# Performance work log

Hardware: AMD Instinct MI355X
Metric: run time of the kernel (lower is better)

Reference implementation:

```python
import jax, jax.numpy as jnp
import numpy as np

DIM, HEADS, K = 128, 4, 7
HD = DIM // HEADS


def _nbr_idx(n, k):
    # NATTEN boundary-clamped neighborhood (dilation=1): window start clamped to [0, n-k]
    i = np.arange(n)
    start = np.clip(i - k // 2, 0, n - k)
    idx = start[:, None] + np.arange(k)[None, :]          # (n, k) absolute neighbor index
    rel = idx - i[:, None] + (k - 1)                      # (n, k) index into 2k-1 rpb axis
    return jnp.asarray(idx), jnp.asarray(rel)


def _ln(x, w, b, eps=1e-5):
    mu = jnp.mean(x, -1, keepdims=True)
    var = jnp.var(x, -1, keepdims=True)
    return (x - mu) * jax.lax.rsqrt(var + eps) * w + b


def setup_inputs() -> dict:
    key = jax.random.key(0)
    ks = jax.random.split(key, 16)
    B, H, W, C = 1, 128, 128, DIM
    f = jax.random.normal
    inp = {
        'x': f(ks[0], (B, H, W, C), jnp.float32),
        'y': f(ks[1], (B, H, W, C), jnp.float32),
        'qv_w': f(ks[2], (2 * C, C), jnp.float32) * 0.02,
        'qv_b': jnp.zeros((2 * C,), jnp.float32),
        'k_w': f(ks[3], (C, C), jnp.float32) * 0.02,
        'k_b': jnp.zeros((C,), jnp.float32),
        'rpb': f(ks[4], (HEADS, 2 * K - 1, 2 * K - 1), jnp.float32) * 0.02,
        'proj_w': f(ks[5], (C, C), jnp.float32) * 0.02,
        'proj_b': jnp.zeros((C,), jnp.float32),
        'n1_w': jnp.ones((C,), jnp.float32),
        'n1_b': jnp.zeros((C,), jnp.float32),
        'n2_w': jnp.ones((C,), jnp.float32),
        'n2_b': jnp.zeros((C,), jnp.float32),
        'fc1_w': f(ks[6], (4 * C, C), jnp.float32) * 0.02,
        'fc1_b': jnp.zeros((4 * C,), jnp.float32),
        'fc2_w': f(ks[7], (C, 4 * C), jnp.float32) * 0.02,
        'fc2_b': jnp.zeros((C,), jnp.float32),
    }
    return inp


def _block(x, y, qv_w, qv_b, k_w, k_b, rpb, proj_w, proj_b,
           n1_w, n1_b, n2_w, n2_b, fc1_w, fc1_b, fc2_w, fc2_b):
    B, H, W, C = x.shape
    scale = HD ** -0.5
    # ---- CrossNat2D attention on norm1(x) vs y ----
    xn = _ln(x, n1_w, n1_b)
    qv = xn @ qv_w.T + qv_b                               # (B,H,W,2C)
    q = qv[..., :C].reshape(B, H, W, HEADS, HD) * scale
    v = qv[..., C:].reshape(B, H, W, HEADS, HD)
    k = (y @ k_w.T + k_b).reshape(B, H, W, HEADS, HD)

    idx_h, rel_h = _nbr_idx(H, K)
    idx_w, rel_w = _nbr_idx(W, K)
    # gather neighborhoods: (B, H, K, W, K, HEADS, HD)
    k_nbr = k[:, idx_h][:, :, :, idx_w]
    v_nbr = v[:, idx_h][:, :, :, idx_w]

    # attention logits over KxK neighborhood
    attn = jnp.einsum('bijhd,biajchd->bijhac', q, k_nbr)  # (B,H,W,heads,K,K)
    bias = rpb[:, rel_h][..., rel_w]                      # (heads,H,K,W,K)
    attn = attn + jnp.transpose(bias, (1, 3, 0, 2, 4))    # broadcast over B
    attn = jax.nn.softmax(attn.reshape(B, H, W, HEADS, K * K), axis=-1)
    attn = attn.reshape(B, H, W, HEADS, K, K)

    out = jnp.einsum('bijhac,biajchd->bijhd', attn, v_nbr).reshape(B, H, W, C)
    out = out @ proj_w.T + proj_b

    x = x + out
    # ---- MLP ----
    h = _ln(x, n2_w, n2_b) @ fc1_w.T + fc1_b
    h = jax.nn.gelu(h, approximate=False) @ fc2_w.T + fc2_b
    return x + h


def reference(x, y, qv_w, qv_b, k_w, k_b, rpb, proj_w, proj_b,
              n1_w, n1_b, n2_w, n2_b, fc1_w, fc1_b, fc2_w, fc2_b):
    return _block(x, y, qv_w, qv_b, k_w, k_b, rpb, proj_w, proj_b,
                  n1_w, n1_b, n2_w, n2_b, fc1_w, fc1_b, fc2_w, fc2_b)
```

## Files before the change

### kernel.cpp

```cpp
#include <hip/hip_runtime.h>
#include <hip/hip_bf16.h>


#define N_PIX 16384
#define C 128
#define HEADS 4
#define HD 32
#define HW 128

typedef __hip_bfloat16 bf16;
typedef __attribute__((ext_vector_type(8))) short bf16x8;
typedef __attribute__((ext_vector_type(4))) float f32x4;

__device__ __forceinline__ short f2bs(float f) {
    bf16 h = __float2bfloat16(f);
    return (short)__bfloat16_as_ushort(h);
}
__device__ __forceinline__ float bs2f(short s) {
    __hip_bfloat16_raw r; r.x = (unsigned short)s;
    return __bfloat162float(__hip_bfloat16(r));
}
__device__ __forceinline__ float gelu_f(float v) {
    const float z = 1.5957691216f * (v + 0.044715f * v * v * v);
    return v / (1.f + __expf(-z));
}

__global__ __launch_bounds__(256) void k_wconv(
    const float* __restrict__ qv_w, const float* __restrict__ k_w,
    const float* __restrict__ proj_w, const float* __restrict__ fc1_w,
    const float* __restrict__ fc2_w,
    short* __restrict__ wqv, short* __restrict__ wk, short* __restrict__ wproj,
    short* __restrict__ wfc1, short* __restrict__ wfc2) {
    const int i = blockIdx.x * 256 + threadIdx.x;
    if (i < 32768) wqv[i] = f2bs(qv_w[i]);
    if (i < 16384) { wk[i] = f2bs(k_w[i]); wproj[i] = f2bs(proj_w[i]); }
    if (i < 65536) { wfc1[i] = f2bs(fc1_w[i]); wfc2[i] = f2bs(fc2_w[i]); }
}

__global__ __launch_bounds__(512, 6) void k_qkv(
    const float* __restrict__ x, const float* __restrict__ y,
    const short* __restrict__ wqv, const float* __restrict__ qv_b,
    const short* __restrict__ wk, const float* __restrict__ k_b,
    const float* __restrict__ n1_w, const float* __restrict__ n1_b,
    bf16* __restrict__ qb, bf16* __restrict__ vb, bf16* __restrict__ kb) {
    __shared__ float xr[32][132];
    __shared__ short xn[32][136];
    __shared__ short yb[32][136];
    __shared__ float muA[32], riA[32];
    const int t = threadIdx.x;
    const int pix0 = (blockIdx.x & 7) * 2048 + (blockIdx.x >> 3) * 32;
    for (int e = t; e < 32 * 128; e += 512) {
        const int r = e >> 7, c = e & 127;
        xr[r][c] = x[(pix0 + r) * C + c];
        yb[r][c] = f2bs(y[(pix0 + r) * C + c]);
    }
    __syncthreads();
    if (t < 256) {
        const int r = t >> 3, s = t & 7;
        float sm = 0.f, sq = 0.f;
        for (int i = 0; i < 16; i++) { float v = xr[r][s * 16 + i]; sm += v; sq += v * v; }
        for (int m = 1; m < 8; m <<= 1) { sm += __shfl_xor(sm, m, 64); sq += __shfl_xor(sq, m, 64); }
        if (s == 0) {
            const float mu = sm * (1.f / 128.f);
            const float var = sq * (1.f / 128.f) - mu * mu;
            muA[r] = mu; riA[r] = rsqrtf(var + 1e-5f);
        }
    }
    __syncthreads();
    for (int e = t; e < 32 * 128; e += 512) {
        const int r = e >> 7, c = e & 127;
        xn[r][c] = f2bs((xr[r][c] - muA[r]) * riA[r] * n1_w[c] + n1_b[c]);
    }
    __syncthreads();
    const int wave = t >> 6, lane = t & 63, quad = lane >> 4, l15 = lane & 15;
    const int mt = wave & 1, wv = wave >> 1;
    const float scale = 0.1767766952966369f;
    {
        bf16x8 aA[4];
#pragma unroll
        for (int kt = 0; kt < 4; kt++)
            aA[kt] = *(const bf16x8*)&xn[mt * 16 + l15][kt * 32 + quad * 8];
#pragma unroll
        for (int s = 0; s < 4; s++) {
            const int n = (wv * 4 + s) * 16 + l15;
            f32x4 acc = {0.f, 0.f, 0.f, 0.f};
#pragma unroll
            for (int kt = 0; kt < 4; kt++) {
                bf16x8 b = *(const bf16x8*)&wqv[n * C + kt * 32 + quad * 8];
                acc = __builtin_amdgcn_mfma_f32_16x16x32_bf16(aA[kt], b, acc, 0, 0, 0);
            }
            const float bias = qv_b[n];
#pragma unroll
            for (int r = 0; r < 4; r++) {
                const int m = mt * 16 + quad * 4 + r;
                const float v = acc[r] + bias;
                if (n < C) qb[(pix0 + m) * C + n] = __float2bfloat16(v * scale);
                else       vb[(pix0 + m) * C + (n - C)] = __float2bfloat16(v);
            }
        }
    }
    {
        bf16x8 aY[4];
#pragma unroll
        for (int kt = 0; kt < 4; kt++)
            aY[kt] = *(const bf16x8*)&yb[mt * 16 + l15][kt * 32 + quad * 8];
        const int n0 = (wv * 2) * 16 + l15, n1 = (wv * 2 + 1) * 16 + l15;
        f32x4 a0 = {0.f, 0.f, 0.f, 0.f}, a1 = {0.f, 0.f, 0.f, 0.f};
#pragma unroll
        for (int kt = 0; kt < 4; kt++) {
            bf16x8 b0 = *(const bf16x8*)&wk[n0 * C + kt * 32 + quad * 8];
            bf16x8 b1 = *(const bf16x8*)&wk[n1 * C + kt * 32 + quad * 8];
            a0 = __builtin_amdgcn_mfma_f32_16x16x32_bf16(aY[kt], b0, a0, 0, 0, 0);
            a1 = __builtin_amdgcn_mfma_f32_16x16x32_bf16(aY[kt], b1, a1, 0, 0, 0);
        }
        const float b0s = k_b[n0], b1s = k_b[n1];
#pragma unroll
        for (int r = 0; r < 4; r++) {
            const int m = mt * 16 + quad * 4 + r;
            kb[(pix0 + m) * C + n0] = __float2bfloat16(a0[r] + b0s);
            kb[(pix0 + m) * C + n1] = __float2bfloat16(a1[r] + b1s);
        }
    }
}

__global__ __launch_bounds__(256) void k_fam(
    const bf16* __restrict__ qb, const bf16* __restrict__ kb,
    const bf16* __restrict__ vb, const float* __restrict__ rpb,
    const float* __restrict__ x,
    const short* __restrict__ wproj, const float* __restrict__ proj_b,
    const float* __restrict__ n2_w, const float* __restrict__ n2_b,
    const short* __restrict__ wfc1, const float* __restrict__ fc1_b,
    const short* __restrict__ wfc2, const float* __restrict__ fc2_b,
    float* __restrict__ out) {
    __shared__ short KP[13200];
    __shared__ short Vl[13200];
    __shared__ float muA[16], riA[16];
    short* const Pm  = KP;
    short* const aoL = KP + 8704;
    short* const x1b = KP + 10880;
    short* const hb  = Vl;
    short* const xnb = Vl + 8320;
    const int t = threadIdx.x;
    const int h = t >> 6, lane = t & 63, quad = lane >> 4, l15 = lane & 15;
    const int s_ = blockIdx.x >> 3;
    const int i0 = ((blockIdx.x & 7) * 4 + (s_ >> 5)) * 4;
    const int j0 = (s_ & 31) * 4;
    const int rs = min(max(i0 - 3, 0), 118);
    const int cs = min(max(j0 - 3, 0), 118);
    for (int u = t; u < 100 * 16 * 2; u += 256) {
        const int tv = (u >= 1600) ? 1 : 0;
        const int uu = tv ? u - 1600 : u;
        const int r = uu >> 4, seg = uu & 15;
        const size_t g = (size_t)((rs + r / 10) * HW + cs + r % 10) * C + seg * 8;
        const uint4 d = *(const uint4*)((tv ? vb : kb) + g);
        *(uint4*)&(tv ? Vl : KP)[r * 132 + seg * 8] = d;
    }
    __syncthreads();
    const int pA = (i0 + (l15 >> 2)) * HW + j0 + (l15 & 3);
    const bf16x8 aQ = *(const bf16x8*)(qb + (size_t)pA * C + h * HD + quad * 8);
    f32x4 S[7];
    int aiL[7], ajL[7]; bool inb[7];
#pragma unroll
    for (int nt = 0; nt < 7; nt++) {
        const int nb = nt * 16 + l15;
        aiL[nt] = rs + nb / 10;
        ajL[nt] = cs + nb % 10;
        inb[nt] = nb < 100;
        const bf16x8 bK = *(const bf16x8*)&KP[(nt * 16 + l15) * 132 + h * HD + quad * 8];
        f32x4 z = {0.f, 0.f, 0.f, 0.f};
        S[nt] = __builtin_amdgcn_mfma_f32_16x16x32_bf16(aQ, bK, z, 0, 0, 0);
    }
    const float* rpbh = rpb + h * 169;
    float smx[4];
#pragma unroll
    for (int r = 0; r < 4; r++) {
        const int m = quad * 4 + r;
        const int i = i0 + (m >> 2), j = j0 + (m & 3);
        const int shi = min(max(i - 3, 0), 121);
        const int swj = min(max(j - 3, 0), 121);
        float best = -1e30f;
#pragma unroll
        for (int nt = 0; nt < 7; nt++) {
            const int ai = aiL[nt], aj = ajL[nt];
            const bool valid = inb[nt] & (ai >= shi) & (ai <= shi + 6) & (aj >= swj) & (aj <= swj + 6);
            const int ri = min(max(ai - i + 6, 0), 12);
            const int rj = min(max(aj - j + 6, 0), 12);
            const float v = valid ? (S[nt][r] + rpbh[ri * 13 + rj]) : -1e30f;
            S[nt][r] = v;
            best = fmaxf(best, v);
        }
        for (int msk = 1; msk < 16; msk <<= 1) best = fmaxf(best, __shfl_xor(best, msk, 64));
        float s = 0.f;
#pragma unroll
        for (int nt = 0; nt < 7; nt++) {
            const float e = __expf(S[nt][r] - best);
            S[nt][r] = e;
            s += e;
        }
        for (int msk = 1; msk < 16; msk <<= 1) s += __shfl_xor(s, msk, 64);
        smx[r] = 1.f / s;
    }
    __syncthreads();
#pragma unroll
    for (int r = 0; r < 4; r++) {
        short* prow = &Pm[(h * 16 + quad * 4 + r) * 136];
#pragma unroll
        for (int nt = 0; nt < 7; nt++)
            prow[nt * 16 + l15] = f2bs(S[nt][r] * smx[r]);
        prow[112 + l15] = 0;
    }
    __syncthreads();
    f32x4 O0 = {0.f, 0.f, 0.f, 0.f}, O1 = {0.f, 0.f, 0.f, 0.f};
#pragma unroll
    for (int kt = 0; kt < 4; kt++) {
        const bf16x8 aP = *(const bf16x8*)&Pm[(h * 16 + l15) * 136 + kt * 32 + quad * 8];
#pragma unroll
        for (int nt2 = 0; nt2 < 2; nt2++) {
            bf16x8 bV;
            const int ch = h * HD + nt2 * 16 + l15;
#pragma unroll
            for (int jj = 0; jj < 8; jj++) {
                const int nbr = kt * 32 + quad * 8 + jj;
                bV[jj] = (nbr < 100) ? Vl[nbr * 132 + ch] : (short)0;
            }
            if (nt2 == 0) O0 = __builtin_amdgcn_mfma_f32_16x16x32_bf16(aP, bV, O0, 0, 0, 0);
            else          O1 = __builtin_amdgcn_mfma_f32_16x16x32_bf16(aP, bV, O1, 0, 0, 0);
        }
    }
#pragma unroll
    for (int r = 0; r < 4; r++) {
        const int m = quad * 4 + r;
        aoL[m * 136 + h * HD + l15] = f2bs(O0[r]);
        aoL[m * 136 + h * HD + 16 + l15] = f2bs(O1[r]);
    }
    __syncthreads();
    {
        bf16x8 aO[4];
#pragma unroll
        for (int kt = 0; kt < 4; kt++)
            aO[kt] = *(const bf16x8*)&aoL[l15 * 136 + kt * 32 + quad * 8];
        const int n0 = h * 16 + l15, n1 = (h + 4) * 16 + l15;
        f32x4 a0 = {0.f, 0.f, 0.f, 0.f}, a1 = {0.f, 0.f, 0.f, 0.f};
#pragma unroll
        for (int kt = 0; kt < 4; kt++) {
            bf16x8 b0 = *(const bf16x8*)&wproj[n0 * C + kt * 32 + quad * 8];
            bf16x8 b1 = *(const bf16x8*)&wproj[n1 * C + kt * 32 + quad * 8];
            a0 = __builtin_amdgcn_mfma_f32_16x16x32_bf16(aO[kt], b0, a0, 0, 0, 0);
            a1 = __builtin_amdgcn_mfma_f32_16x16x32_bf16(aO[kt], b1, a1, 0, 0, 0);
        }
        const float b0s = proj_b[n0], b1s = proj_b[n1];
#pragma unroll
        for (int r = 0; r < 4; r++) {
            const int m = quad * 4 + r;
            const int p = (i0 + (m >> 2)) * HW + j0 + (m & 3);
            x1b[m * 136 + n0] = f2bs(x[(size_t)p * C + n0] + a0[r] + b0s);
            x1b[m * 136 + n1] = f2bs(x[(size_t)p * C + n1] + a1[r] + b1s);
        }
    }
    __syncthreads();
    if (t < 128) {
        const int r = t >> 3, s = t & 7;
        float sm = 0.f, sq = 0.f;
        for (int i = 0; i < 16; i++) { float v = bs2f(x1b[r * 136 + s * 16 + i]); sm += v; sq += v * v; }
        for (int m = 1; m < 8; m <<= 1) { sm += __shfl_xor(sm, m, 64); sq += __shfl_xor(sq, m, 64); }
        if (s == 0) {
            const float mu = sm * (1.f / 128.f);
            const float var = sq * (1.f / 128.f) - mu * mu;
            muA[r] = mu; riA[r] = rsqrtf(var + 1e-5f);
        }
    }
    __syncthreads();
    for (int e = t; e < 16 * 128; e += 256) {
        const int r = e >> 7, c = e & 127;
        xnb[r * 136 + c] = f2bs((bs2f(x1b[r * 136 + c]) - muA[r]) * riA[r] * n2_w[c] + n2_b[c]);
    }
    __syncthreads();
    {
        bf16x8 aX[4];
#pragma unroll
        for (int kt = 0; kt < 4; kt++)
            aX[kt] = *(const bf16x8*)&xnb[l15 * 136 + kt * 32 + quad * 8];
#pragma unroll
        for (int a = 0; a < 4; a++) {
            const int n0 = (h + 8 * a) * 16 + l15, n1 = (h + 8 * a + 4) * 16 + l15;
            f32x4 a0 = {0.f, 0.f, 0.f, 0.f}, a1 = {0.f, 0.f, 0.f, 0.f};
#pragma unroll
            for (int kt = 0; kt < 4; kt++) {
                bf16x8 b0 = *(const bf16x8*)&wfc1[n0 * C + kt * 32 + quad * 8];
                bf16x8 b1 = *(const bf16x8*)&wfc1[n1 * C + kt * 32 + quad * 8];
                a0 = __builtin_amdgcn_mfma_f32_16x16x32_bf16(aX[kt], b0, a0, 0, 0, 0);
                a1 = __builtin_amdgcn_mfma_f32_16x16x32_bf16(aX[kt], b1, a1, 0, 0, 0);
            }
            const float b0s = fc1_b[n0], b1s = fc1_b[n1];
#pragma unroll
            for (int r = 0; r < 4; r++) {
                hb[(quad * 4 + r) * 520 + n0] = f2bs(gelu_f(a0[r] + b0s));
                hb[(quad * 4 + r) * 520 + n1] = f2bs(gelu_f(a1[r] + b1s));
            }
        }
    }
    __syncthreads();
    {
        const int n0 = h * 16 + l15, n1 = (h + 4) * 16 + l15;
        f32x4 a0 = {0.f, 0.f, 0.f, 0.f}, a1 = {0.f, 0.f, 0.f, 0.f};
#pragma unroll
        for (int kt = 0; kt < 16; kt++) {
            const bf16x8 aP = *(const bf16x8*)&hb[l15 * 520 + kt * 32 + quad * 8];
            bf16x8 b0 = *(const bf16x8*)&wfc2[n0 * 512 + kt * 32 + quad * 8];
            bf16x8 b1 = *(const bf16x8*)&wfc2[n1 * 512 + kt * 32 + quad * 8];
            a0 = __builtin_amdgcn_mfma_f32_16x16x32_bf16(aP, b0, a0, 0, 0, 0);
            a1 = __builtin_amdgcn_mfma_f32_16x16x32_bf16(aP, b1, a1, 0, 0, 0);
        }
        const float b0s = fc2_b[n0], b1s = fc2_b[n1];
#pragma unroll
        for (int r = 0; r < 4; r++) {
            const int m = quad * 4 + r;
            const int p = (i0 + (m >> 2)) * HW + j0 + (m & 3);
            out[(size_t)p * C + n0] = a0[r] + b0s + bs2f(x1b[m * 136 + n0]);
            out[(size_t)p * C + n1] = a1[r] + b1s + bs2f(x1b[m * 136 + n1]);
        }
    }
}

extern "C" void kernel_launch(void* const* d_in, const int* in_sizes, int n_in,
                              void* d_out, int out_size, void* d_ws, size_t ws_size,
                              hipStream_t stream) {
    const float* x      = (const float*)d_in[0];
    const float* y      = (const float*)d_in[1];
    const float* qv_w   = (const float*)d_in[2];
    const float* qv_b   = (const float*)d_in[3];
    const float* k_w    = (const float*)d_in[4];
    const float* k_b    = (const float*)d_in[5];
    const float* rpb    = (const float*)d_in[6];
    const float* proj_w = (const float*)d_in[7];
    const float* proj_b = (const float*)d_in[8];
    const float* n1_w   = (const float*)d_in[9];
    const float* n1_b   = (const float*)d_in[10];
    const float* n2_w   = (const float*)d_in[11];
    const float* n2_b   = (const float*)d_in[12];
    const float* fc1_w  = (const float*)d_in[13];
    const float* fc1_b  = (const float*)d_in[14];
    const float* fc2_w  = (const float*)d_in[15];
    const float* fc2_b  = (const float*)d_in[16];
    float* out = (float*)d_out;

    bf16* qb  = (bf16*)d_ws;
    bf16* vb  = qb + (size_t)N_PIX * C;
    bf16* kb  = vb + (size_t)N_PIX * C;
    short* wqv  = (short*)(kb + (size_t)N_PIX * C);
    short* wk   = wqv + 32768;
    short* wproj= wk + 16384;
    short* wfc1 = wproj + 16384;
    short* wfc2 = wfc1 + 65536;

    k_wconv<<<256, 256, 0, stream>>>(qv_w, k_w, proj_w, fc1_w, fc2_w,
                                     wqv, wk, wproj, wfc1, wfc2);
    k_qkv<<<N_PIX / 32, 512, 0, stream>>>(x, y, wqv, qv_b, wk, k_b, n1_w, n1_b, qb, vb, kb);
    k_fam<<<1024, 256, 0, stream>>>(qb, kb, vb, rpb, x, wproj, proj_b, n2_w, n2_b,
                                    wfc1, fc1_b, wfc2, fc2_b, out);
}
```

Baseline: 175.5 us.

## Double per-block pixel tiles in QKV and fused attention-MLP kernels

The QKV projection block now processes 64 pixels instead of 32, and the fused attention/MLP block processes an 8x4 query tile with 512 threads instead of 4x4 with 256. The larger attention tile shares a 14x10 K/V halo across twice the queries, which cuts redundant halo loads and amortises weight fetches per block. In exchange each query scores 144 neighbour slots instead of 112, which is more wasted MFMA work. The grids shrink to 256 and 512 blocks, which lowers occupancy and parallelism on a large GPU. Shared memory is re-laid out, and an extra barrier is added before attention outputs overwrite the probability buffer.

```diff
diff --git a/kernel.cpp b/kernel.cpp
--- a/kernel.cpp
+++ b/kernel.cpp
@@ -37,25 +37,25 @@
     if (i < 65536) { wfc1[i] = f2bs(fc1_w[i]); wfc2[i] = f2bs(fc2_w[i]); }
 }
 
-__global__ __launch_bounds__(512, 6) void k_qkv(
+__global__ __launch_bounds__(512, 2) void k_qkv(
     const float* __restrict__ x, const float* __restrict__ y,
     const short* __restrict__ wqv, const float* __restrict__ qv_b,
     const short* __restrict__ wk, const float* __restrict__ k_b,
     const float* __restrict__ n1_w, const float* __restrict__ n1_b,
     bf16* __restrict__ qb, bf16* __restrict__ vb, bf16* __restrict__ kb) {
-    __shared__ float xr[32][132];
-    __shared__ short xn[32][136];
-    __shared__ short yb[32][136];
-    __shared__ float muA[32], riA[32];
+    __shared__ float xr[64][132];
+    __shared__ short xn[64][136];
+    __shared__ short yb[64][136];
+    __shared__ float muA[64], riA[64];
     const int t = threadIdx.x;
-    const int pix0 = (blockIdx.x & 7) * 2048 + (blockIdx.x >> 3) * 32;
-    for (int e = t; e < 32 * 128; e += 512) {
+    const int pix0 = (blockIdx.x & 7) * 2048 + (blockIdx.x >> 3) * 64;
+    for (int e = t; e < 64 * 128; e += 512) {
         const int r = e >> 7, c = e & 127;
         xr[r][c] = x[(pix0 + r) * C + c];
         yb[r][c] = f2bs(y[(pix0 + r) * C + c]);
     }
     __syncthreads();
-    if (t < 256) {
+    {
         const int r = t >> 3, s = t & 7;
         float sm = 0.f, sq = 0.f;
         for (int i = 0; i < 16; i++) { float v = xr[r][s * 16 + i]; sm += v; sq += v * v; }
@@ -67,13 +67,13 @@
         }
     }
     __syncthreads();
-    for (int e = t; e < 32 * 128; e += 512) {
+    for (int e = t; e < 64 * 128; e += 512) {
         const int r = e >> 7, c = e & 127;
         xn[r][c] = f2bs((xr[r][c] - muA[r]) * riA[r] * n1_w[c] + n1_b[c]);
     }
     __syncthreads();
     const int wave = t >> 6, lane = t & 63, quad = lane >> 4, l15 = lane & 15;
-    const int mt = wave & 1, wv = wave >> 1;
+    const int mt = wave >> 1, half = wave & 1;
     const float scale = 0.1767766952966369f;
     {
         bf16x8 aA[4];
@@ -81,8 +81,8 @@
         for (int kt = 0; kt < 4; kt++)
             aA[kt] = *(const bf16x8*)&xn[mt * 16 + l15][kt * 32 + quad * 8];
 #pragma unroll
-        for (int s = 0; s < 4; s++) {
-            const int n = (wv * 4 + s) * 16 + l15;
+        for (int s = 0; s < 8; s++) {
+            const int n = (half + 2 * s) * 16 + l15;
             f32x4 acc = {0.f, 0.f, 0.f, 0.f};
 #pragma unroll
             for (int kt = 0; kt < 4; kt++) {
@@ -104,26 +104,30 @@
 #pragma unroll
         for (int kt = 0; kt < 4; kt++)
             aY[kt] = *(const bf16x8*)&yb[mt * 16 + l15][kt * 32 + quad * 8];
-        const int n0 = (wv * 2) * 16 + l15, n1 = (wv * 2 + 1) * 16 + l15;
-        f32x4 a0 = {0.f, 0.f, 0.f, 0.f}, a1 = {0.f, 0.f, 0.f, 0.f};
-#pragma unroll
-        for (int kt = 0; kt < 4; kt++) {
-            bf16x8 b0 = *(const bf16x8*)&wk[n0 * C + kt * 32 + quad * 8];
-            bf16x8 b1 = *(const bf16x8*)&wk[n1 * C + kt * 32 + quad * 8];
-            a0 = __builtin_amdgcn_mfma_f32_16x16x32_bf16(aY[kt], b0, a0, 0, 0, 0);
-            a1 = __builtin_amdgcn_mfma_f32_16x16x32_bf16(aY[kt], b1, a1, 0, 0, 0);
-        }
-        const float b0s = k_b[n0], b1s = k_b[n1];
-#pragma unroll
-        for (int r = 0; r < 4; r++) {
-            const int m = mt * 16 + quad * 4 + r;
-            kb[(pix0 + m) * C + n0] = __float2bfloat16(a0[r] + b0s);
-            kb[(pix0 + m) * C + n1] = __float2bfloat16(a1[r] + b1s);
-        }
-    }
-}
-
-__global__ __launch_bounds__(256) void k_fam(
+#pragma unroll
+        for (int s = 0; s < 2; s++) {
+            const int n0 = (half + 2 * (2 * s)) * 16 + l15;
+            const int n1 = (half + 2 * (2 * s + 1)) * 16 + l15;
+            f32x4 a0 = {0.f, 0.f, 0.f, 0.f}, a1 = {0.f, 0.f, 0.f, 0.f};
+#pragma unroll
+            for (int kt = 0; kt < 4; kt++) {
+                bf16x8 b0 = *(const bf16x8*)&wk[n0 * C + kt * 32 + quad * 8];
+                bf16x8 b1 = *(const bf16x8*)&wk[n1 * C + kt * 32 + quad * 8];
+                a0 = __builtin_amdgcn_mfma_f32_16x16x32_bf16(aY[kt], b0, a0, 0, 0, 0);
+                a1 = __builtin_amdgcn_mfma_f32_16x16x32_bf16(aY[kt], b1, a1, 0, 0, 0);
+            }
+            const float b0s = k_b[n0], b1s = k_b[n1];
+#pragma unroll
+            for (int r = 0; r < 4; r++) {
+                const int m = mt * 16 + quad * 4 + r;
+                kb[(pix0 + m) * C + n0] = __float2bfloat16(a0[r] + b0s);
+                kb[(pix0 + m) * C + n1] = __float2bfloat16(a1[r] + b1s);
+            }
+        }
+    }
+}
+
+__global__ __launch_bounds__(512, 2) void k_fam(
     const bf16* __restrict__ qb, const bf16* __restrict__ kb,
     const bf16* __restrict__ vb, const float* __restrict__ rpb,
     const float* __restrict__ x,
@@ -132,57 +136,56 @@
     const short* __restrict__ wfc1, const float* __restrict__ fc1_b,
     const short* __restrict__ wfc2, const float* __restrict__ fc2_b,
     float* __restrict__ out) {
-    __shared__ short KP[13200];
-    __shared__ short Vl[13200];
-    __shared__ float muA[16], riA[16];
+    __shared__ short KP[19008];
+    __shared__ short Vl[19008];
+    __shared__ float muA[32], riA[32];
     short* const Pm  = KP;
-    short* const aoL = KP + 8704;
-    short* const x1b = KP + 10880;
+    short* const aoL = KP;
+    short* const x1b = KP + 4352;
+    short* const xnb = KP + 8704;
     short* const hb  = Vl;
-    short* const xnb = Vl + 8320;
     const int t = threadIdx.x;
-    const int h = t >> 6, lane = t & 63, quad = lane >> 4, l15 = lane & 15;
+    const int wave = t >> 6, lane = t & 63, quad = lane >> 4, l15 = lane & 15;
+    const int h = wave & 3, mt = wave >> 2;
     const int s_ = blockIdx.x >> 3;
-    const int i0 = ((blockIdx.x & 7) * 4 + (s_ >> 5)) * 4;
+    const int i0 = ((blockIdx.x & 7) * 2 + (s_ >> 5)) * 8;
     const int j0 = (s_ & 31) * 4;
-    const int rs = min(max(i0 - 3, 0), 118);
+    const int rs = min(max(i0 - 3, 0), 114);
     const int cs = min(max(j0 - 3, 0), 118);
-    for (int u = t; u < 100 * 16 * 2; u += 256) {
-        const int tv = (u >= 1600) ? 1 : 0;
-        const int uu = tv ? u - 1600 : u;
+    for (int u = t; u < 140 * 16 * 2; u += 512) {
+        const int tv = (u >= 2240) ? 1 : 0;
+        const int uu = tv ? u - 2240 : u;
         const int r = uu >> 4, seg = uu & 15;
         const size_t g = (size_t)((rs + r / 10) * HW + cs + r % 10) * C + seg * 8;
         const uint4 d = *(const uint4*)((tv ? vb : kb) + g);
         *(uint4*)&(tv ? Vl : KP)[r * 132 + seg * 8] = d;
     }
     __syncthreads();
-    const int pA = (i0 + (l15 >> 2)) * HW + j0 + (l15 & 3);
+    const int mA = mt * 16 + l15;
+    const int pA = (i0 + (mA >> 2)) * HW + j0 + (mA & 3);
     const bf16x8 aQ = *(const bf16x8*)(qb + (size_t)pA * C + h * HD + quad * 8);
-    f32x4 S[7];
-    int aiL[7], ajL[7]; bool inb[7];
-#pragma unroll
-    for (int nt = 0; nt < 7; nt++) {
-        const int nb = nt * 16 + l15;
-        aiL[nt] = rs + nb / 10;
-        ajL[nt] = cs + nb % 10;
-        inb[nt] = nb < 100;
+    f32x4 S[9];
+#pragma unroll
+    for (int nt = 0; nt < 9; nt++) {
         const bf16x8 bK = *(const bf16x8*)&KP[(nt * 16 + l15) * 132 + h * HD + quad * 8];
         f32x4 z = {0.f, 0.f, 0.f, 0.f};
         S[nt] = __builtin_amdgcn_mfma_f32_16x16x32_bf16(aQ, bK, z, 0, 0, 0);
     }
+    const int nbL = l15;
     const float* rpbh = rpb + h * 169;
     float smx[4];
 #pragma unroll
     for (int r = 0; r < 4; r++) {
-        const int m = quad * 4 + r;
+        const int m = mt * 16 + quad * 4 + r;
         const int i = i0 + (m >> 2), j = j0 + (m & 3);
         const int shi = min(max(i - 3, 0), 121);
         const int swj = min(max(j - 3, 0), 121);
         float best = -1e30f;
 #pragma unroll
-        for (int nt = 0; nt < 7; nt++) {
-            const int ai = aiL[nt], aj = ajL[nt];
-            const bool valid = inb[nt] & (ai >= shi) & (ai <= shi + 6) & (aj >= swj) & (aj <= swj + 6);
+        for (int nt = 0; nt < 9; nt++) {
+            const int nb = nt * 16 + nbL;
+            const int ai = rs + nb / 10, aj = cs + nb % 10;
+            const bool valid = (nb < 140) & (ai >= shi) & (ai <= shi + 6) & (aj >= swj) & (aj <= swj + 6);
             const int ri = min(max(ai - i + 6, 0), 12);
             const int rj = min(max(aj - j + 6, 0), 12);
             const float v = valid ? (S[nt][r] + rpbh[ri * 13 + rj]) : -1e30f;
@@ -192,7 +195,7 @@
         for (int msk = 1; msk < 16; msk <<= 1) best = fmaxf(best, __shfl_xor(best, msk, 64));
         float s = 0.f;
 #pragma unroll
-        for (int nt = 0; nt < 7; nt++) {
+        for (int nt = 0; nt < 9; nt++) {
             const float e = __expf(S[nt][r] - best);
             S[nt][r] = e;
             s += e;
@@ -203,17 +206,16 @@
     __syncthreads();
 #pragma unroll
     for (int r = 0; r < 4; r++) {
-        short* prow = &Pm[(h * 16 + quad * 4 + r) * 136];
-#pragma unroll
-        for (int nt = 0; nt < 7; nt++)
+        short* prow = &Pm[(wave * 16 + quad * 4 + r) * 144];
+#pragma unroll
+        for (int nt = 0; nt < 9; nt++)
             prow[nt * 16 + l15] = f2bs(S[nt][r] * smx[r]);
-        prow[112 + l15] = 0;
     }
     __syncthreads();
     f32x4 O0 = {0.f, 0.f, 0.f, 0.f}, O1 = {0.f, 0.f, 0.f, 0.f};
 #pragma unroll
-    for (int kt = 0; kt < 4; kt++) {
-        const bf16x8 aP = *(const bf16x8*)&Pm[(h * 16 + l15) * 136 + kt * 32 + quad * 8];
+    for (int kt = 0; kt < 5; kt++) {
+        const bf16x8 aP = *(const bf16x8*)&Pm[(wave * 16 + l15) * 144 + kt * 32 + quad * 8];
 #pragma unroll
         for (int nt2 = 0; nt2 < 2; nt2++) {
             bf16x8 bV;
@@ -221,15 +223,16 @@
 #pragma unroll
             for (int jj = 0; jj < 8; jj++) {
                 const int nbr = kt * 32 + quad * 8 + jj;
-                bV[jj] = (nbr < 100) ? Vl[nbr * 132 + ch] : (short)0;
+                bV[jj] = (nbr < 140) ? Vl[nbr * 132 + ch] : (short)0;
             }
             if (nt2 == 0) O0 = __builtin_amdgcn_mfma_f32_16x16x32_bf16(aP, bV, O0, 0, 0, 0);
             else          O1 = __builtin_amdgcn_mfma_f32_16x16x32_bf16(aP, bV, O1, 0, 0, 0);
         }
     }
+    __syncthreads();
 #pragma unroll
     for (int r = 0; r < 4; r++) {
-        const int m = quad * 4 + r;
+        const int m = mt * 16 + quad * 4 + r;
         aoL[m * 136 + h * HD + l15] = f2bs(O0[r]);
         aoL[m * 136 + h * HD + 16 + l15] = f2bs(O1[r]);
     }
@@ -238,7 +241,7 @@
         bf16x8 aO[4];
 #pragma unroll
         for (int kt = 0; kt < 4; kt++)
-            aO[kt] = *(const bf16x8*)&aoL[l15 * 136 + kt * 32 + quad * 8];
+            aO[kt] = *(const bf16x8*)&aoL[(mt * 16 + l15) * 136 + kt * 32 + quad * 8];
         const int n0 = h * 16 + l15, n1 = (h + 4) * 16 + l15;
         f32x4 a0 = {0.f, 0.f, 0.f, 0.f}, a1 = {0.f, 0.f, 0.f, 0.f};
 #pragma unroll
@@ -251,14 +254,14 @@
         const float b0s = proj_b[n0], b1s = proj_b[n1];
 #pragma unroll
         for (int r = 0; r < 4; r++) {
-            const int m = quad * 4 + r;
+            const int m = mt * 16 + quad * 4 + r;
             const int p = (i0 + (m >> 2)) * HW + j0 + (m & 3);
             x1b[m * 136 + n0] = f2bs(x[(size_t)p * C + n0] + a0[r] + b0s);
             x1b[m * 136 + n1] = f2bs(x[(size_t)p * C + n1] + a1[r] + b1s);
         }
     }
     __syncthreads();
-    if (t < 128) {
+    if (t < 256) {
         const int r = t >> 3, s = t & 7;
         float sm = 0.f, sq = 0.f;
         for (int i = 0; i < 16; i++) { float v = bs2f(x1b[r * 136 + s * 16 + i]); sm += v; sq += v * v; }
@@ -270,7 +273,7 @@
         }
     }
     __syncthreads();
-    for (int e = t; e < 16 * 128; e += 256) {
+    for (int e = t; e < 32 * 128; e += 512) {
         const int r = e >> 7, c = e & 127;
         xnb[r * 136 + c] = f2bs((bs2f(x1b[r * 136 + c]) - muA[r]) * riA[r] * n2_w[c] + n2_b[c]);
     }
@@ -279,7 +282,7 @@
         bf16x8 aX[4];
 #pragma unroll
         for (int kt = 0; kt < 4; kt++)
-            aX[kt] = *(const bf16x8*)&xnb[l15 * 136 + kt * 32 + quad * 8];
+            aX[kt] = *(const bf16x8*)&xnb[(mt * 16 + l15) * 136 + kt * 32 + quad * 8];
 #pragma unroll
         for (int a = 0; a < 4; a++) {
             const int n0 = (h + 8 * a) * 16 + l15, n1 = (h + 8 * a + 4) * 16 + l15;
@@ -294,8 +297,9 @@
             const float b0s = fc1_b[n0], b1s = fc1_b[n1];
 #pragma unroll
             for (int r = 0; r < 4; r++) {
-                hb[(quad * 4 + r) * 520 + n0] = f2bs(gelu_f(a0[r] + b0s));
-                hb[(quad * 4 + r) * 520 + n1] = f2bs(gelu_f(a1[r] + b1s));
+                const int m = mt * 16 + quad * 4 + r;
+                hb[m * 520 + n0] = f2bs(gelu_f(a0[r] + b0s));
+                hb[m * 520 + n1] = f2bs(gelu_f(a1[r] + b1s));
             }
         }
     }
@@ -305,7 +309,7 @@
         f32x4 a0 = {0.f, 0.f, 0.f, 0.f}, a1 = {0.f, 0.f, 0.f, 0.f};
 #pragma unroll
         for (int kt = 0; kt < 16; kt++) {
-            const bf16x8 aP = *(const bf16x8*)&hb[l15 * 520 + kt * 32 + quad * 8];
+            const bf16x8 aP = *(const bf16x8*)&hb[(mt * 16 + l15) * 520 + kt * 32 + quad * 8];
             bf16x8 b0 = *(const bf16x8*)&wfc2[n0 * 512 + kt * 32 + quad * 8];
             bf16x8 b1 = *(const bf16x8*)&wfc2[n1 * 512 + kt * 32 + quad * 8];
             a0 = __builtin_amdgcn_mfma_f32_16x16x32_bf16(aP, b0, a0, 0, 0, 0);
@@ -314,7 +318,7 @@
         const float b0s = fc2_b[n0], b1s = fc2_b[n1];
 #pragma unroll
         for (int r = 0; r < 4; r++) {
-            const int m = quad * 4 + r;
+            const int m = mt * 16 + quad * 4 + r;
             const int p = (i0 + (m >> 2)) * HW + j0 + (m & 3);
             out[(size_t)p * C + n0] = a0[r] + b0s + bs2f(x1b[m * 136 + n0]);
             out[(size_t)p * C + n1] = a1[r] + b1s + bs2f(x1b[m * 136 + n1]);
@@ -355,7 +359,7 @@
 
     k_wconv<<<256, 256, 0, stream>>>(qv_w, k_w, proj_w, fc1_w, fc2_w,
                                      wqv, wk, wproj, wfc1, wfc2);
-    k_qkv<<<N_PIX / 32, 512, 0, stream>>>(x, y, wqv, qv_b, wk, k_b, n1_w, n1_b, qb, vb, kb);
-    k_fam<<<1024, 256, 0, stream>>>(qb, kb, vb, rpb, x, wproj, proj_b, n2_w, n2_b,
-                                    wfc1, fc1_b, wfc2, fc2_b, out);
-}
+    k_qkv<<<256, 512, 0, stream>>>(x, y, wqv, qv_b, wk, k_b, n1_w, n1_b, qb, vb, kb);
+    k_fam<<<512, 512, 0, stream>>>(qb, kb, vb, rpb, x, wproj, proj_b, n2_w, n2_b,
+                                   wfc1, fc1_b, wfc2, fc2_b, out);
+}
```

Measured after the change: 165.9 us. 5.5% less time.
